# Optimization experiments

Measured on AMD Instinct MI355X. Metric: run time of the kernel, lower is better.

## Reference

```python
import jax, jax.numpy as jnp
import numpy as np

T, B, IN_DIM = 8192, 4, 512
D_V, D_K, CHUNK = 512, 64, 128
EPS = 1e-8


def setup_inputs() -> dict:
    key = jax.random.key(0)
    ks = jax.random.split(key, 9)
    s = 0.02
    return {
        "x": jax.random.normal(ks[0], (T, B, IN_DIM), jnp.float32),
        "Wv": jax.random.normal(ks[1], (D_V, IN_DIM), jnp.float32) * s,
        "bv": jnp.zeros((D_V,), jnp.float32),
        "Wk": jax.random.normal(ks[2], (D_K, IN_DIM), jnp.float32) * s,
        "bk": jnp.zeros((D_K,), jnp.float32),
        "Wq": jax.random.normal(ks[3], (D_K, IN_DIM), jnp.float32) * s,
        "bq": jnp.zeros((D_K,), jnp.float32),
        "Wa": jax.random.normal(ks[4], (D_K, IN_DIM), jnp.float32) * s,
        "ba": jnp.zeros((D_K,), jnp.float32),
    }


def reference(x, Wv, bv, Wk, bk, Wq, bq, Wa, ba):
    # Projections: x (T, B, in_dim)
    v = x @ Wv.T + bv                      # (T, B, d)
    k = x @ Wk.T + bk                      # (T, B, n)
    q = x @ Wq.T + bq                      # (T, B, n)
    alpha = jax.nn.sigmoid(x @ Wa.T + ba)  # (T, B, n) decay gates

    Tt, Bb = x.shape[0], x.shape[1]
    C = CHUNK
    nC = Tt // C  # T assumed divisible by chunk size

    def to_chunks(a):
        return a.reshape(nC, C, Bb, a.shape[-1])

    vs, ks_, qs, als = to_chunks(v), to_chunks(k), to_chunks(q), to_chunks(alpha)
    causal = jnp.tril(jnp.ones((C, C), dtype=bool))  # (C, C)

    def body(S, inp):
        v_ch, k_ch, q_ch, a_ch = inp  # each (C, B, .)
        # Cumulative decay product within chunk (clamped as in the original)
        p = jnp.cumprod(jnp.maximum(a_ch, EPS), axis=0)      # (C, B, n)
        q_t = q_ch * p                                        # (C, B, n)
        k_t = k_ch / (p + EPS)                                # (C, B, n)
        # Intra-chunk causal attention scores
        A = jnp.einsum('tbn,sbn->bts', q_t, k_t)              # (B, C, C)
        A = jnp.where(causal[None, :, :], A, jnp.zeros((), A.dtype))
        y = jnp.einsum('bts,sbd->tbd', A, v_ch)               # intra-chunk
        y = y + jnp.einsum('bdn,tbn->tbd', S, q_t)            # cross-chunk carry
        # State update to end of chunk
        p_end = p[-1]                                         # (B, n)
        S_writes = jnp.einsum('tbd,tbn->bdn', v_ch, k_t * p_end[None, :, :])
        S_new = S * p_end[:, None, :] + S_writes              # (B, d, n)
        return S_new, y

    S0 = jnp.zeros((Bb, D_V, D_K), x.dtype)
    _, ys = jax.lax.scan(body, S0, (vs, ks_, qs, als))        # ys: (nC, C, B, d)
    return ys.reshape(Tt, Bb, D_V)
```

## Files before the change

### kernel.cpp

```cpp
#include <hip/hip_runtime.h>
#include <math.h>

#define T_DIM 8192
#define B_DIM 4
#define INDIM 512
#define DV 512
#define DK 64
#define CHUNK 128
#define NCH (T_DIM / CHUNK)
#define ROWS (T_DIM * B_DIM)
#define NPAD 768
#define KCAT 192
#define EPSF 1e-8f

typedef float float4_t __attribute__((ext_vector_type(4)));
typedef short short8_t __attribute__((ext_vector_type(8)));
typedef _Float16 half8_t __attribute__((ext_vector_type(8)));

__device__ inline unsigned short f2bf(float f) {
  unsigned int u = __float_as_uint(f);
  unsigned int r = (u + 0x7fffu + ((u >> 16) & 1u)) >> 16;
  return (unsigned short)r;
}
__device__ inline float bf2f(unsigned short h) {
  return __uint_as_float(((unsigned int)h) << 16);
}
__device__ inline unsigned short f2h(float f) {
  _Float16 h = (_Float16)f;
  unsigned short u;
  __builtin_memcpy(&u, &h, 2);
  return u;
}

__device__ inline void gload16(const void* g, void* l) {
  __builtin_amdgcn_global_load_lds(
      (const __attribute__((address_space(1))) void*)g,
      (__attribute__((address_space(3))) void*)l, 16, 0, 0);
}

__global__ __launch_bounds__(256) void cast_kernel(
    const float* __restrict__ x,
    const float* __restrict__ Wv, const float* __restrict__ Wk,
    const float* __restrict__ Wq, const float* __restrict__ Wa,
    const float* __restrict__ bv, const float* __restrict__ bk,
    const float* __restrict__ bq, const float* __restrict__ ba,
    unsigned short* __restrict__ xh, unsigned short* __restrict__ wh,
    float* __restrict__ bcat)
{
  if (blockIdx.x < 16384) {
    const size_t i4 = ((size_t)blockIdx.x * 256 + threadIdx.x) * 4;
    const float4 v = *(const float4*)&x[i4];
    ushort4 h;
    h.x = f2h(v.x); h.y = f2h(v.y); h.z = f2h(v.z); h.w = f2h(v.w);
    *(ushort4*)&xh[i4] = h;
  } else {
    const int t = (blockIdx.x - 16384) * 256 + threadIdx.x;
    const size_t i4 = (size_t)t * 4;
    const int row = (int)(i4 >> 9);
    const int col = (int)(i4 & 511);
    float4 v = {0.f, 0.f, 0.f, 0.f};
    if (row < 512)      v = *(const float4*)&Wv[(size_t)row * INDIM + col];
    else if (row < 576) v = *(const float4*)&Wk[(size_t)(row - 512) * INDIM + col];
    else if (row < 640) v = *(const float4*)&Wq[(size_t)(row - 576) * INDIM + col];
    else if (row < 704) v = *(const float4*)&Wa[(size_t)(row - 640) * INDIM + col];
    ushort4 h;
    h.x = f2h(v.x); h.y = f2h(v.y); h.z = f2h(v.z); h.w = f2h(v.w);
    *(ushort4*)&wh[i4] = h;
    if (t < NPAD) {
      float b = 0.f;
      if (t < 512)      b = bv[t];
      else if (t < 576) b = bk[t - 512];
      else if (t < 640) b = bq[t - 576];
      else if (t < 704) b = ba[t - 640];
      bcat[t] = b;
    }
  }
}

__global__ __launch_bounds__(256) void proj_mfma_kernel(
    const unsigned short* __restrict__ xh, const unsigned short* __restrict__ wh,
    const float* __restrict__ bcat,
    unsigned short* __restrict__ Bt_h, unsigned short* __restrict__ Bt_l,
    float* __restrict__ k_ws, float* __restrict__ q_ws,
    float* __restrict__ a_ws)
{
  __shared__ __align__(16) _Float16 Ah[3][128 * 32];
  __shared__ __align__(16) _Float16 Bh[3][128 * 32];

  const int d     = blockIdx.x;
  const int grp   = d >> 3;
  const int ytile = (d & 7) * 32 + grp / 6;
  const int xtile = grp % 6;
  const int r0 = ytile * 128;
  const int c0 = xtile * 128;

  const int tid  = threadIdx.x;
  const int wave = tid >> 6, lane = tid & 63;
  const int wm   = (wave & 1) * 64, wn = (wave >> 1) * 64;
  const int fm   = lane & 15;
  const int fk   = (lane >> 4) * 8;
  const int g    = lane >> 4;

  float4_t acc[4][4];
#pragma unroll
  for (int i = 0; i < 4; ++i)
#pragma unroll
    for (int j = 0; j < 4; ++j) acc[i][j] = (float4_t)0.0f;

  const int srow = tid >> 2;
  const int scol = (tid & 3) * 8;

  const unsigned short* pA0 = xh + (size_t)(r0 + srow) * INDIM + scol;
  const unsigned short* pA1 = xh + (size_t)(r0 + 64 + srow) * INDIM + scol;
  const unsigned short* pB0 = wh + (size_t)(c0 + srow) * INDIM + scol;
  const unsigned short* pB1 = wh + (size_t)(c0 + 64 + srow) * INDIM + scol;

  auto stage = [&](int buf, int k0) {
    gload16(pA0 + k0, &Ah[buf][tid * 8]);
    gload16(pA1 + k0, &Ah[buf][(256 + tid) * 8]);
    gload16(pB0 + k0, &Bh[buf][tid * 8]);
    gload16(pB1 + k0, &Bh[buf][(256 + tid) * 8]);
  };

  auto compute = [&](int buf) {
    half8_t a[4], b[4];
#pragma unroll
    for (int i = 0; i < 4; ++i)
      a[i] = *(const half8_t*)&Ah[buf][(wm + i * 16 + fm) * 32 + fk];
#pragma unroll
    for (int j = 0; j < 4; ++j)
      b[j] = *(const half8_t*)&Bh[buf][(wn + j * 16 + fm) * 32 + fk];
    __builtin_amdgcn_s_setprio(1);
#pragma unroll
    for (int i = 0; i < 4; ++i)
#pragma unroll
      for (int j = 0; j < 4; ++j)
        acc[i][j] = __builtin_amdgcn_mfma_f32_16x16x32_f16(a[i], b[j], acc[i][j], 0, 0, 0);
    __builtin_amdgcn_s_setprio(0);
  };

  stage(0, 0);
  stage(1, 32);
  int cur = 0;
  for (int t = 0; t < 14; ++t) {
    stage((cur + 2) % 3, (t + 2) * 32);
    asm volatile("s_waitcnt vmcnt(8)" ::: "memory");
    __builtin_amdgcn_s_barrier();
    compute(cur);
    __builtin_amdgcn_s_barrier();
    cur = (cur + 1) % 3;
  }
  asm volatile("s_waitcnt vmcnt(4)" ::: "memory");
  __builtin_amdgcn_s_barrier();
  compute(cur);
  cur = (cur + 1) % 3;
  asm volatile("s_waitcnt vmcnt(0)" ::: "memory");
  __builtin_amdgcn_s_barrier();
  compute(cur);

  if (xtile < 4) {
    unsigned int* Thl = (unsigned int*)&Ah[0][0];
    const int t0 = r0 >> 2;
    const int cb0 = (t0 >> 7) * 4;
    const int s0 = t0 & 127;
    __syncthreads();
    for (int bb = 0; bb < 4; ++bb) {
#pragma unroll
      for (int j = 0; j < 4; ++j) {
        const int d_loc = wn + j * 16 + fm;
        const float bias = bcat[c0 + d_loc];
#pragma unroll
        for (int i = 0; i < 4; ++i) {
          const int trow = (wm >> 2) + i * 4 + g;
          const float val = acc[i][j][bb] + bias;
          const unsigned short h = f2bf(val);
          const unsigned short l = f2bf(val - bf2f(h));
          Thl[d_loc * 34 + trow] = (unsigned int)h | ((unsigned int)l << 16);
        }
      }
      __syncthreads();
#pragma unroll
      for (int q2 = 0; q2 < 4; ++q2) {
        const int task = q2 * 256 + tid;
        const int dd = task >> 3;
        const int tq = task & 7;
        const unsigned int* p = &Thl[dd * 34 + tq * 4];
        const unsigned int w0 = p[0], w1 = p[1], w2 = p[2], w3 = p[3];
        ushort4 hh, ll;
        hh.x = (unsigned short)w0; ll.x = (unsigned short)(w0 >> 16);
        hh.y = (unsigned short)w1; ll.y = (unsigned short)(w1 >> 16);
        hh.z = (unsigned short)w2; ll.z = (unsigned short)(w2 >> 16);
        hh.w = (unsigned short)w3; ll.w = (unsigned short)(w3 >> 16);
        const size_t oa = ((size_t)(cb0 + bb) * DV + c0 + dd) * CHUNK + s0 + tq * 4;
        *(ushort4*)&Bt_h[oa] = hh;
        *(ushort4*)&Bt_l[oa] = ll;
      }
      __syncthreads();
    }
  } else {
#pragma unroll
    for (int j = 0; j < 4; ++j) {
      const int col = c0 + wn + j * 16 + fm;
      if (col >= 704) continue;
      const float bias = bcat[col];
#pragma unroll
      for (int i = 0; i < 4; ++i) {
#pragma unroll
        for (int r = 0; r < 4; ++r) {
          const int row = r0 + wm + i * 16 + g * 4 + r;
          const float val = acc[i][j][r] + bias;
          if (col < 576) {
            k_ws[(size_t)row * DK + col - 512] = val;
          } else if (col < 640) {
            q_ws[(size_t)row * DK + col - 576] = val;
          } else {
            a_ws[(size_t)row * DK + col - 640] = 1.0f / (1.0f + expf(-val));
          }
        }
      }
    }
  }
}

__global__ __launch_bounds__(512) void prep_kernel(
    const float* __restrict__ a_ws, const float* __restrict__ k_ws,
    const float* __restrict__ q_ws,
    unsigned short* __restrict__ Acat_h, unsigned short* __restrict__ Acat_l,
    unsigned short* __restrict__ kT_h, unsigned short* __restrict__ kT_l,
    float* __restrict__ pend)
{
  __shared__ float pal[CHUNK][DK];
  __shared__ __align__(16) unsigned short Aq_h[128 * 64];
  __shared__ __align__(16) unsigned short Aq_l[128 * 64];
  __shared__ __align__(16) unsigned short Bk_h[128 * 64];
  __shared__ __align__(16) unsigned short Bk_l[128 * 64];

  const int c = blockIdx.x, b = blockIdx.y;
  const int cb = c * B_DIM + b;
  const int tid = threadIdx.x;
  const int wave = tid >> 6, lane = tid & 63;
  const int wm = (wave & 1) * 64, wn = (wave >> 1) * 32;
  const int fm = lane & 15;
  const int fk = (lane >> 4) * 8;
  const int g  = lane >> 4;

#pragma unroll
  for (int i = 0; i < 4; ++i) {
    const int f = (i * 512 + tid) * 4;
    const int t = f >> 6, n0 = f & 63;
    const float4 av = *(const float4*)&a_ws[(size_t)(c * CHUNK + t) * 256 + b * 64 + n0];
    *(float4*)&pal[t][n0] = av;
  }
  __syncthreads();

  if (tid < 64) {
    float p = 1.0f;
#pragma unroll 4
    for (int t = 0; t < CHUNK; ++t) {
      p *= fmaxf(pal[t][tid], EPSF);
      pal[t][tid] = p;
    }
    pend[c * 256 + b * 64 + tid] = p;
  }
  __syncthreads();

#pragma unroll
  for (int i = 0; i < 4; ++i) {
    const int f = (i * 512 + tid) * 4;
    const int t = f >> 6, n0 = f & 63;
    const float4 qv = *(const float4*)&q_ws[(size_t)(c * CHUNK + t) * 256 + b * 64 + n0];
    const size_t qa = ((size_t)cb * CHUNK + t) * KCAT + 128 + n0;
    float q0 = qv.x * pal[t][n0 + 0];
    float q1 = qv.y * pal[t][n0 + 1];
    float q2 = qv.z * pal[t][n0 + 2];
    float q3 = qv.w * pal[t][n0 + 3];
    ushort4 h, l;
    h.x = f2bf(q0); l.x = f2bf(q0 - bf2f(h.x));
    h.y = f2bf(q1); l.y = f2bf(q1 - bf2f(h.y));
    h.z = f2bf(q2); l.z = f2bf(q2 - bf2f(h.z));
    h.w = f2bf(q3); l.w = f2bf(q3 - bf2f(h.w));
    *(ushort4*)&Acat_h[qa] = h;
    *(ushort4*)&Acat_l[qa] = l;
    const int wi = t * 64 + (n0 ^ ((t & 7) << 3));
    *(ushort4*)&Aq_h[wi] = h;
    *(ushort4*)&Aq_l[wi] = l;
  }

#pragma unroll
  for (int i = 0; i < 4; ++i) {
    const int f = (i * 512 + tid) * 4;
    const int t = f >> 6, n0 = f & 63;
    const float4 kv = *(const float4*)&k_ws[(size_t)(c * CHUNK + t) * 256 + b * 64 + n0];
    float k0 = kv.x / (pal[t][n0 + 0] + EPSF);
    float k1 = kv.y / (pal[t][n0 + 1] + EPSF);
    float k2 = kv.z / (pal[t][n0 + 2] + EPSF);
    float k3 = kv.w / (pal[t][n0 + 3] + EPSF);
    ushort4 h, l;
    h.x = f2bf(k0); l.x = f2bf(k0 - bf2f(h.x));
    h.y = f2bf(k1); l.y = f2bf(k1 - bf2f(h.y));
    h.z = f2bf(k2); l.z = f2bf(k2 - bf2f(h.z));
    h.w = f2bf(k3); l.w = f2bf(k3 - bf2f(h.w));
    const int wi = t * 64 + (n0 ^ ((t & 7) << 3));
    *(ushort4*)&Bk_h[wi] = h;
    *(ushort4*)&Bk_l[wi] = l;
  }
  __syncthreads();

#pragma unroll
  for (int it = 0; it < 2; ++it) {
    const int task = it * 512 + tid;
    const int n  = task >> 4;
    const int tg = task & 15;
    ushort4 h0, h1, l0, l1;
    unsigned short hh[8], ll[8];
#pragma unroll
    for (int e = 0; e < 8; ++e) {
      const int wi = (tg * 8 + e) * 64 + (n ^ (e << 3));
      hh[e] = Bk_h[wi];
      ll[e] = Bk_l[wi];
    }
    h0.x = hh[0]; h0.y = hh[1]; h0.z = hh[2]; h0.w = hh[3];
    h1.x = hh[4]; h1.y = hh[5]; h1.z = hh[6]; h1.w = hh[7];
    l0.x = ll[0]; l0.y = ll[1]; l0.z = ll[2]; l0.w = ll[3];
    l1.x = ll[4]; l1.y = ll[5]; l1.z = ll[6]; l1.w = ll[7];
    const size_t oa = ((size_t)cb * DK + n) * CHUNK + tg * 8;
    *(ushort4*)&kT_h[oa]     = h0;
    *(ushort4*)&kT_h[oa + 4] = h1;
    *(ushort4*)&kT_l[oa]     = l0;
    *(ushort4*)&kT_l[oa + 4] = l1;
  }

  float4_t acc[4][2];
#pragma unroll
  for (int i = 0; i < 4; ++i)
#pragma unroll
    for (int j = 0; j < 2; ++j) acc[i][j] = (float4_t)0.0f;

#pragma unroll
  for (int ksub = 0; ksub < 2; ++ksub) {
    short8_t a_hi[4], a_lo[4], b_hi[2], b_lo[2];
#pragma unroll
    for (int i = 0; i < 4; ++i) {
      const int r = wm + i * 16 + fm;
      const int ar = r * 64 + ((ksub * 32 + fk) ^ ((r & 7) << 3));
      a_hi[i] = *(const short8_t*)&Aq_h[ar];
      a_lo[i] = *(const short8_t*)&Aq_l[ar];
    }
#pragma unroll
    for (int j = 0; j < 2; ++j) {
      const int r = wn + j * 16 + fm;
      const int br = r * 64 + ((ksub * 32 + fk) ^ ((r & 7) << 3));
      b_hi[j] = *(const short8_t*)&Bk_h[br];
      b_lo[j] = *(const short8_t*)&Bk_l[br];
    }
    __builtin_amdgcn_s_setprio(1);
#pragma unroll
    for (int i = 0; i < 4; ++i)
#pragma unroll
      for (int j = 0; j < 2; ++j) {
        acc[i][j] = __builtin_amdgcn_mfma_f32_16x16x32_bf16(a_hi[i], b_hi[j], acc[i][j], 0, 0, 0);
        acc[i][j] = __builtin_amdgcn_mfma_f32_16x16x32_bf16(a_lo[i], b_hi[j], acc[i][j], 0, 0, 0);
        acc[i][j] = __builtin_amdgcn_mfma_f32_16x16x32_bf16(a_hi[i], b_lo[j], acc[i][j], 0, 0, 0);
      }
    __builtin_amdgcn_s_setprio(0);
  }

#pragma unroll
  for (int j = 0; j < 2; ++j) {
    const int s = wn + j * 16 + fm;
#pragma unroll
    for (int i = 0; i < 4; ++i) {
#pragma unroll
      for (int r = 0; r < 4; ++r) {
        const int t = wm + i * 16 + g * 4 + r;
        const float vv = (s <= t) ? acc[i][j][r] : 0.0f;
        const unsigned short h = f2bf(vv);
        const size_t oa = ((size_t)cb * CHUNK + t) * KCAT + s;
        Acat_h[oa] = h;
        Acat_l[oa] = f2bf(vv - bf2f(h));
      }
    }
  }
}

__global__ __launch_bounds__(256) void wchunk_mfma_kernel(
    const unsigned short* __restrict__ Bt_h, const unsigned short* __restrict__ Bt_l,
    const unsigned short* __restrict__ kT_h, const unsigned short* __restrict__ kT_l,
    const float* __restrict__ pend, float* __restrict__ W_ws)
{
  __shared__ __align__(16) unsigned short Ah[128 * 32];
  __shared__ __align__(16) unsigned short Al[128 * 32];
  __shared__ __align__(16) unsigned short Kh[64 * 128];
  __shared__ __align__(16) unsigned short Kl[64 * 128];

  const int bd = blockIdx.x;
  const int cb = (bd >> 5) * 8 + (bd & 7);
  const int dt = (bd >> 3) & 3;
  const int c = cb >> 2, b = cb & 3;
  (void)c; (void)b;
  const int tid  = threadIdx.x;
  const int wave = tid >> 6, lane = tid & 63;
  const int wm   = (wave & 1) * 64;
  const int wn   = (wave >> 1) * 32;
  const int fm   = lane & 15;
  const int fk   = (lane >> 4) * 8;

  const unsigned short* Ab_h = Bt_h + ((size_t)cb * DV + dt * 128) * CHUNK;
  const unsigned short* Ab_l = Bt_l + ((size_t)cb * DV + dt * 128) * CHUNK;
  const unsigned short* Kb_h = kT_h + (size_t)cb * DK * CHUNK;
  const unsigned short* Kb_l = kT_l + (size_t)cb * DK * CHUNK;

#pragma unroll
  for (int it = 0; it < 4; ++it) {
    const int tk = it * 256 + tid;
    const int n = tk >> 4, slot = tk & 15;
    gload16(&Kb_h[(size_t)n * CHUNK + ((slot ^ (n & 15)) << 3)], &Kh[tk * 8]);
    gload16(&Kb_l[(size_t)n * CHUNK + ((slot ^ (n & 15)) << 3)], &Kl[tk * 8]);
  }

  float4_t acc[4][2];
#pragma unroll
  for (int i = 0; i < 4; ++i)
#pragma unroll
    for (int j = 0; j < 2; ++j) acc[i][j] = (float4_t)0.0f;

  for (int ks = 0; ks < 4; ++ks) {
    const int k0 = ks * 32;
#pragma unroll
    for (int q = 0; q < 2; ++q) {
      const int flat = (q * 256 + tid) * 8;
      const int row = flat >> 5, col = flat & 31;
      gload16(&Ab_h[(size_t)row * CHUNK + k0 + col], &Ah[flat]);
      gload16(&Ab_l[(size_t)row * CHUNK + k0 + col], &Al[flat]);
    }
    __syncthreads();

    short8_t a_hi[4], a_lo[4], b_hi[2], b_lo[2];
#pragma unroll
    for (int i = 0; i < 4; ++i) {
      const int ar = (wm + i * 16 + fm) * 32 + fk;
      a_hi[i] = *(const short8_t*)&Ah[ar];
      a_lo[i] = *(const short8_t*)&Al[ar];
    }
#pragma unroll
    for (int j = 0; j < 2; ++j) {
      const int n = wn + j * 16 + fm;
      const int slot = (k0 + fk) >> 3;
      const int addr = n * CHUNK + ((slot ^ (n & 15)) << 3);
      b_hi[j] = *(const short8_t*)&Kh[addr];
      b_lo[j] = *(const short8_t*)&Kl[addr];
    }
#pragma unroll
    for (int i = 0; i < 4; ++i)
#pragma unroll
      for (int j = 0; j < 2; ++j) {
        acc[i][j] = __builtin_amdgcn_mfma_f32_16x16x32_bf16(a_hi[i], b_hi[j], acc[i][j], 0, 0, 0);
        acc[i][j] = __builtin_amdgcn_mfma_f32_16x16x32_bf16(a_lo[i], b_hi[j], acc[i][j], 0, 0, 0);
        acc[i][j] = __builtin_amdgcn_mfma_f32_16x16x32_bf16(a_hi[i], b_lo[j], acc[i][j], 0, 0, 0);
      }
    __syncthreads();
  }

#pragma unroll
  for (int j = 0; j < 2; ++j) {
    const int n = wn + j * 16 + fm;
    const float pj = pend[(cb >> 2) * 256 + (cb & 3) * 64 + n];
#pragma unroll
    for (int i = 0; i < 4; ++i) {
#pragma unroll
      for (int r = 0; r < 4; ++r) {
        const int dd = dt * 128 + wm + i * 16 + (lane >> 4) * 4 + r;
        W_ws[((size_t)cb * DV + dd) * DK + n] = acc[i][j][r] * pj;
      }
    }
  }
}

__global__ __launch_bounds__(256) void scan_kernel(
    const float* __restrict__ W_ws, const float* __restrict__ pend,
    unsigned short* __restrict__ Sh, unsigned short* __restrict__ Sl)
{
  const int flat = blockIdx.x * 256 + threadIdx.x;
  const int n = flat & 63;
  const int bd = flat >> 6;
  const int b = bd >> 9;
  float s = 0.0f;
  for (int c = 0; c < NCH; ++c) {
    const int off = c * 131072 + flat;
    const float w = W_ws[off];
    const unsigned short h = f2bf(s);
    Sh[off] = h;
    Sl[off] = f2bf(s - bf2f(h));
    s = s * pend[c * 256 + b * 64 + n] + w;
  }
}

__global__ __launch_bounds__(256) void out_mfma_kernel(
    const unsigned short* __restrict__ Acat_h, const unsigned short* __restrict__ Acat_l,
    const unsigned short* __restrict__ Bt_h, const unsigned short* __restrict__ Bt_l,
    const unsigned short* __restrict__ Sh, const unsigned short* __restrict__ Sl,
    float* __restrict__ out)
{
  __shared__ __align__(16) unsigned short Ah[128 * 64];
  __shared__ __align__(16) unsigned short Al[128 * 64];
  __shared__ __align__(16) unsigned short Bh[128 * 64];
  __shared__ __align__(16) unsigned short Bl[128 * 64];

  const int bd = blockIdx.x;
  const int cb = (bd >> 5) * 8 + (bd & 7);
  const int nt = (bd >> 3) & 3;
  const int c = cb >> 2, b = cb & 3;
  const int tid  = threadIdx.x;
  const int wave = tid >> 6, lane = tid & 63;
  const int wm   = (wave & 1) * 64, wn = (wave >> 1) * 64;
  const int fm   = lane & 15;
  const int fk   = (lane >> 4) * 8;

  const unsigned short* Ab_h = Acat_h + (size_t)cb * CHUNK * KCAT;
  const unsigned short* Ab_l = Acat_l + (size_t)cb * CHUNK * KCAT;
  const unsigned short* Bb_h = Bt_h + ((size_t)cb * DV + nt * 128) * CHUNK;
  const unsigned short* Bb_l = Bt_l + ((size_t)cb * DV + nt * 128) * CHUNK;
  const unsigned short* Sb_h = Sh + ((size_t)cb * DV + nt * 128) * DK;
  const unsigned short* Sb_l = Sl + ((size_t)cb * DV + nt * 128) * DK;

  const int srow = tid >> 3;
  const int scolB = (tid & 7) * 16;
  const int sc = (scolB ^ ((srow & 7) << 4)) >> 1;
  const int sdst = srow * 64 + (scolB >> 1);

  float4_t acc[4][4];
#pragma unroll
  for (int i = 0; i < 4; ++i)
#pragma unroll
    for (int j = 0; j < 4; ++j) acc[i][j] = (float4_t)0.0f;

  for (int ks = 0; ks < 3; ++ks) {
    const int k0 = ks * 64;
#pragma unroll
    for (int q = 0; q < 4; ++q) {
      const int row = q * 32 + srow;
      const int dst = q * 2048 + sdst;
      gload16(&Ab_h[(size_t)row * KCAT + k0 + sc], &Ah[dst]);
      gload16(&Ab_l[(size_t)row * KCAT + k0 + sc], &Al[dst]);
      if (ks < 2) {
        gload16(&Bb_h[(size_t)row * CHUNK + k0 + sc], &Bh[dst]);
        gload16(&Bb_l[(size_t)row * CHUNK + k0 + sc], &Bl[dst]);
      } else {
        gload16(&Sb_h[(size_t)row * DK + sc], &Bh[dst]);
        gload16(&Sb_l[(size_t)row * DK + sc], &Bl[dst]);
      }
    }
    __syncthreads();

#pragma unroll
    for (int ksub = 0; ksub < 2; ++ksub) {
      short8_t a_hi[4], a_lo[4], b_hi[4], b_lo[4];
#pragma unroll
      for (int i = 0; i < 4; ++i) {
        const int r = wm + i * 16 + fm;
        const int ar = r * 64 + ((ksub * 32 + fk) ^ ((r & 7) << 3));
        a_hi[i] = *(const short8_t*)&Ah[ar];
        a_lo[i] = *(const short8_t*)&Al[ar];
      }
#pragma unroll
      for (int j = 0; j < 4; ++j) {
        const int r = wn + j * 16 + fm;
        const int br = r * 64 + ((ksub * 32 + fk) ^ ((r & 7) << 3));
        b_hi[j] = *(const short8_t*)&Bh[br];
        b_lo[j] = *(const short8_t*)&Bl[br];
      }
      __builtin_amdgcn_s_setprio(1);
#pragma unroll
      for (int i = 0; i < 4; ++i)
#pragma unroll
        for (int j = 0; j < 4; ++j) {
          acc[i][j] = __builtin_amdgcn_mfma_f32_16x16x32_bf16(a_hi[i], b_hi[j], acc[i][j], 0, 0, 0);
          acc[i][j] = __builtin_amdgcn_mfma_f32_16x16x32_bf16(a_lo[i], b_hi[j], acc[i][j], 0, 0, 0);
          acc[i][j] = __builtin_amdgcn_mfma_f32_16x16x32_bf16(a_hi[i], b_lo[j], acc[i][j], 0, 0, 0);
        }
      __builtin_amdgcn_s_setprio(0);
    }
    __syncthreads();
  }

#pragma unroll
  for (int j = 0; j < 4; ++j) {
    const int d = nt * 128 + wn + j * 16 + fm;
#pragma unroll
    for (int i = 0; i < 4; ++i) {
#pragma unroll
      for (int r = 0; r < 4; ++r) {
        const int t = c * CHUNK + wm + i * 16 + (lane >> 4) * 4 + r;
        out[((size_t)t * B_DIM + b) * DV + d] = acc[i][j][r];
      }
    }
  }
}

extern "C" void kernel_launch(void* const* d_in, const int* in_sizes, int n_in,
                              void* d_out, int out_size, void* d_ws, size_t ws_size,
                              hipStream_t stream)
{
  const float* x  = (const float*)d_in[0];
  const float* Wv = (const float*)d_in[1];
  const float* bv = (const float*)d_in[2];
  const float* Wk = (const float*)d_in[3];
  const float* bk = (const float*)d_in[4];
  const float* Wq = (const float*)d_in[5];
  const float* bq = (const float*)d_in[6];
  const float* Wa = (const float*)d_in[7];
  const float* ba = (const float*)d_in[8];
  float* out = (float*)d_out;

  float* ws   = (float*)d_ws;
  unsigned short* Bt_h = (unsigned short*)ws;
  unsigned short* Bt_l = Bt_h + (size_t)NCH * B_DIM * DV * CHUNK;
  float* k_ws = ws + (size_t)ROWS * DV;
  float* a_ws = k_ws + (size_t)ROWS * DK;
  float* pend = a_ws + (size_t)ROWS * DK;
  float* W_ws = pend + NCH * B_DIM * DK;
  float* bcat = W_ws + (size_t)NCH * B_DIM * DV * DK;
  unsigned short* Acat_h = (unsigned short*)(bcat + NPAD);
  unsigned short* Acat_l = Acat_h + (size_t)NCH * B_DIM * CHUNK * KCAT;
  unsigned short* uni = Acat_l + (size_t)NCH * B_DIM * CHUNK * KCAT;
  unsigned short* xh = uni;
  unsigned short* wh = xh + (size_t)ROWS * INDIM;
  float* q_ws = (float*)(uni + (size_t)18 * 1024 * 1024);
  unsigned short* kT_h = (unsigned short*)(q_ws + (size_t)ROWS * DK);
  unsigned short* kT_l = kT_h + (size_t)NCH * B_DIM * DK * CHUNK;
  unsigned short* S_h = uni;
  unsigned short* S_l = S_h + (size_t)NCH * B_DIM * DV * DK;

  cast_kernel<<<16384 + 384, 256, 0, stream>>>(
      x, Wv, Wk, Wq, Wa, bv, bk, bq, ba, xh, wh, bcat);
  proj_mfma_kernel<<<(ROWS / 128) * (NPAD / 128), 256, 0, stream>>>(
      xh, wh, bcat, Bt_h, Bt_l, k_ws, q_ws, a_ws);
  prep_kernel<<<dim3(NCH, B_DIM), 512, 0, stream>>>(
      a_ws, k_ws, q_ws, Acat_h, Acat_l, kT_h, kT_l, pend);
  wchunk_mfma_kernel<<<NCH * B_DIM * 4, 256, 0, stream>>>(
      Bt_h, Bt_l, kT_h, kT_l, pend, W_ws);
  scan_kernel<<<(B_DIM * DV * DK) / 256, 256, 0, stream>>>(
      W_ws, pend, S_h, S_l);
  out_mfma_kernel<<<NCH * B_DIM * 4, 256, 0, stream>>>(
      Acat_h, Acat_l, Bt_h, Bt_l, S_h, S_l, out);
}
```

Measured before the change: 260.1 us.

## Fuse fp32-to-fp16 cast of x into projection GEMM's A-tile loader

```diff
diff --git a/kernel.cpp b/kernel.cpp
--- a/kernel.cpp
+++ b/kernel.cpp
@@ -38,47 +38,37 @@
       (__attribute__((address_space(3))) void*)l, 16, 0, 0);
 }
 
-__global__ __launch_bounds__(256) void cast_kernel(
-    const float* __restrict__ x,
+__global__ __launch_bounds__(256) void wcast_kernel(
     const float* __restrict__ Wv, const float* __restrict__ Wk,
     const float* __restrict__ Wq, const float* __restrict__ Wa,
     const float* __restrict__ bv, const float* __restrict__ bk,
     const float* __restrict__ bq, const float* __restrict__ ba,
-    unsigned short* __restrict__ xh, unsigned short* __restrict__ wh,
-    float* __restrict__ bcat)
+    unsigned short* __restrict__ wh, float* __restrict__ bcat)
 {
-  if (blockIdx.x < 16384) {
-    const size_t i4 = ((size_t)blockIdx.x * 256 + threadIdx.x) * 4;
-    const float4 v = *(const float4*)&x[i4];
-    ushort4 h;
-    h.x = f2h(v.x); h.y = f2h(v.y); h.z = f2h(v.z); h.w = f2h(v.w);
-    *(ushort4*)&xh[i4] = h;
-  } else {
-    const int t = (blockIdx.x - 16384) * 256 + threadIdx.x;
-    const size_t i4 = (size_t)t * 4;
-    const int row = (int)(i4 >> 9);
-    const int col = (int)(i4 & 511);
-    float4 v = {0.f, 0.f, 0.f, 0.f};
-    if (row < 512)      v = *(const float4*)&Wv[(size_t)row * INDIM + col];
-    else if (row < 576) v = *(const float4*)&Wk[(size_t)(row - 512) * INDIM + col];
-    else if (row < 640) v = *(const float4*)&Wq[(size_t)(row - 576) * INDIM + col];
-    else if (row < 704) v = *(const float4*)&Wa[(size_t)(row - 640) * INDIM + col];
-    ushort4 h;
-    h.x = f2h(v.x); h.y = f2h(v.y); h.z = f2h(v.z); h.w = f2h(v.w);
-    *(ushort4*)&wh[i4] = h;
-    if (t < NPAD) {
-      float b = 0.f;
-      if (t < 512)      b = bv[t];
-      else if (t < 576) b = bk[t - 512];
-      else if (t < 640) b = bq[t - 576];
-      else if (t < 704) b = ba[t - 640];
-      bcat[t] = b;
-    }
+  const int t = blockIdx.x * 256 + threadIdx.x;
+  const size_t i4 = (size_t)t * 4;
+  const int row = (int)(i4 >> 9);
+  const int col = (int)(i4 & 511);
+  float4 v = {0.f, 0.f, 0.f, 0.f};
+  if (row < 512)      v = *(const float4*)&Wv[(size_t)row * INDIM + col];
+  else if (row < 576) v = *(const float4*)&Wk[(size_t)(row - 512) * INDIM + col];
+  else if (row < 640) v = *(const float4*)&Wq[(size_t)(row - 576) * INDIM + col];
+  else if (row < 704) v = *(const float4*)&Wa[(size_t)(row - 640) * INDIM + col];
+  ushort4 h;
+  h.x = f2h(v.x); h.y = f2h(v.y); h.z = f2h(v.z); h.w = f2h(v.w);
+  *(ushort4*)&wh[i4] = h;
+  if (t < NPAD) {
+    float b = 0.f;
+    if (t < 512)      b = bv[t];
+    else if (t < 576) b = bk[t - 512];
+    else if (t < 640) b = bq[t - 576];
+    else if (t < 704) b = ba[t - 640];
+    bcat[t] = b;
   }
 }
 
 __global__ __launch_bounds__(256) void proj_mfma_kernel(
-    const unsigned short* __restrict__ xh, const unsigned short* __restrict__ wh,
+    const float* __restrict__ x, const unsigned short* __restrict__ wh,
     const float* __restrict__ bcat,
     unsigned short* __restrict__ Bt_h, unsigned short* __restrict__ Bt_l,
     float* __restrict__ k_ws, float* __restrict__ q_ws,
@@ -110,18 +100,38 @@
   const int srow = tid >> 2;
   const int scol = (tid & 3) * 8;
 
-  const unsigned short* pA0 = xh + (size_t)(r0 + srow) * INDIM + scol;
-  const unsigned short* pA1 = xh + (size_t)(r0 + 64 + srow) * INDIM + scol;
+  const float* pX0 = x + (size_t)(r0 + srow) * INDIM + scol;
+  const float* pX1 = x + (size_t)(r0 + 64 + srow) * INDIM + scol;
   const unsigned short* pB0 = wh + (size_t)(c0 + srow) * INDIM + scol;
   const unsigned short* pB1 = wh + (size_t)(c0 + 64 + srow) * INDIM + scol;
 
-  auto stage = [&](int buf, int k0) {
-    gload16(pA0 + k0, &Ah[buf][tid * 8]);
-    gload16(pA1 + k0, &Ah[buf][(256 + tid) * 8]);
+  float4 ra0[4], ra1[4];
+
+  auto loadA = [&](float4* ra, int kt) {
+    const int k0 = kt * 32;
+    ra[0] = *(const float4*)(pX0 + k0);
+    ra[1] = *(const float4*)(pX0 + k0 + 4);
+    ra[2] = *(const float4*)(pX1 + k0);
+    ra[3] = *(const float4*)(pX1 + k0 + 4);
+  };
+  auto writeA = [&](const float4* ra, int buf) {
+    half8_t h0, h1;
+    h0[0] = (_Float16)ra[0].x; h0[1] = (_Float16)ra[0].y;
+    h0[2] = (_Float16)ra[0].z; h0[3] = (_Float16)ra[0].w;
+    h0[4] = (_Float16)ra[1].x; h0[5] = (_Float16)ra[1].y;
+    h0[6] = (_Float16)ra[1].z; h0[7] = (_Float16)ra[1].w;
+    h1[0] = (_Float16)ra[2].x; h1[1] = (_Float16)ra[2].y;
+    h1[2] = (_Float16)ra[2].z; h1[3] = (_Float16)ra[2].w;
+    h1[4] = (_Float16)ra[3].x; h1[5] = (_Float16)ra[3].y;
+    h1[6] = (_Float16)ra[3].z; h1[7] = (_Float16)ra[3].w;
+    *(half8_t*)&Ah[buf][tid * 8] = h0;
+    *(half8_t*)&Ah[buf][(256 + tid) * 8] = h1;
+  };
+  auto stageB = [&](int buf, int kt) {
+    const int k0 = kt * 32;
     gload16(pB0 + k0, &Bh[buf][tid * 8]);
     gload16(pB1 + k0, &Bh[buf][(256 + tid) * 8]);
   };
-
   auto compute = [&](int buf) {
     half8_t a[4], b[4];
 #pragma unroll
@@ -139,24 +149,27 @@
     __builtin_amdgcn_s_setprio(0);
   };
 
-  stage(0, 0);
-  stage(1, 32);
-  int cur = 0;
-  for (int t = 0; t < 14; ++t) {
-    stage((cur + 2) % 3, (t + 2) * 32);
-    asm volatile("s_waitcnt vmcnt(8)" ::: "memory");
-    __builtin_amdgcn_s_barrier();
-    compute(cur);
-    __builtin_amdgcn_s_barrier();
-    cur = (cur + 1) % 3;
-  }
-  asm volatile("s_waitcnt vmcnt(4)" ::: "memory");
-  __builtin_amdgcn_s_barrier();
-  compute(cur);
-  cur = (cur + 1) % 3;
-  asm volatile("s_waitcnt vmcnt(0)" ::: "memory");
-  __builtin_amdgcn_s_barrier();
-  compute(cur);
+  loadA(ra0, 0);
+  stageB(0, 0);
+  loadA(ra1, 1);
+  stageB(1, 1);
+
+#define PSTEP(T, RA)                                                       \
+  {                                                                        \
+    if ((T) < 15) asm volatile("s_waitcnt vmcnt(6)" ::: "memory");         \
+    else          asm volatile("s_waitcnt vmcnt(0)" ::: "memory");         \
+    writeA(RA, (T) % 3);                                                   \
+    if ((T) + 2 < 16) { loadA(RA, (T) + 2); stageB(((T) + 2) % 3, (T) + 2); } \
+    asm volatile("s_waitcnt lgkmcnt(0)" ::: "memory");                     \
+    __builtin_amdgcn_s_barrier();                                          \
+    compute((T) % 3);                                                      \
+    __builtin_amdgcn_s_barrier();                                          \
+  }
+  PSTEP(0, ra0)  PSTEP(1, ra1)  PSTEP(2, ra0)  PSTEP(3, ra1)
+  PSTEP(4, ra0)  PSTEP(5, ra1)  PSTEP(6, ra0)  PSTEP(7, ra1)
+  PSTEP(8, ra0)  PSTEP(9, ra1)  PSTEP(10, ra0) PSTEP(11, ra1)
+  PSTEP(12, ra0) PSTEP(13, ra1) PSTEP(14, ra0) PSTEP(15, ra1)
+#undef PSTEP
 
   if (xtile < 4) {
     unsigned int* Thl = (unsigned int*)&Ah[0][0];
@@ -180,20 +193,25 @@
       }
       __syncthreads();
 #pragma unroll
-      for (int q2 = 0; q2 < 4; ++q2) {
+      for (int q2 = 0; q2 < 2; ++q2) {
         const int task = q2 * 256 + tid;
-        const int dd = task >> 3;
-        const int tq = task & 7;
-        const unsigned int* p = &Thl[dd * 34 + tq * 4];
+        const int dd = task >> 2;
+        const int tq = task & 3;
+        const unsigned int* p = &Thl[dd * 34 + tq * 8];
         const unsigned int w0 = p[0], w1 = p[1], w2 = p[2], w3 = p[3];
-        ushort4 hh, ll;
-        hh.x = (unsigned short)w0; ll.x = (unsigned short)(w0 >> 16);
-        hh.y = (unsigned short)w1; ll.y = (unsigned short)(w1 >> 16);
-        hh.z = (unsigned short)w2; ll.z = (unsigned short)(w2 >> 16);
-        hh.w = (unsigned short)w3; ll.w = (unsigned short)(w3 >> 16);
-        const size_t oa = ((size_t)(cb0 + bb) * DV + c0 + dd) * CHUNK + s0 + tq * 4;
-        *(ushort4*)&Bt_h[oa] = hh;
-        *(ushort4*)&Bt_l[oa] = ll;
+        const unsigned int w4 = p[4], w5 = p[5], w6 = p[6], w7 = p[7];
+        uint4 hv, lv;
+        hv.x = (w0 & 0xffffu) | (w1 << 16);
+        hv.y = (w2 & 0xffffu) | (w3 << 16);
+        hv.z = (w4 & 0xffffu) | (w5 << 16);
+        hv.w = (w6 & 0xffffu) | (w7 << 16);
+        lv.x = (w0 >> 16) | (w1 & 0xffff0000u);
+        lv.y = (w2 >> 16) | (w3 & 0xffff0000u);
+        lv.z = (w4 >> 16) | (w5 & 0xffff0000u);
+        lv.w = (w6 >> 16) | (w7 & 0xffff0000u);
+        const size_t oa = ((size_t)(cb0 + bb) * DV + c0 + dd) * CHUNK + s0 + tq * 8;
+        *(uint4*)&Bt_h[oa] = hv;
+        *(uint4*)&Bt_l[oa] = lv;
       }
       __syncthreads();
     }
@@ -396,8 +414,6 @@
   const int bd = blockIdx.x;
   const int cb = (bd >> 5) * 8 + (bd & 7);
   const int dt = (bd >> 3) & 3;
-  const int c = cb >> 2, b = cb & 3;
-  (void)c; (void)b;
   const int tid  = threadIdx.x;
   const int wave = tid >> 6, lane = tid & 63;
   const int wm   = (wave & 1) * 64;
@@ -623,18 +639,17 @@
   unsigned short* Acat_h = (unsigned short*)(bcat + NPAD);
   unsigned short* Acat_l = Acat_h + (size_t)NCH * B_DIM * CHUNK * KCAT;
   unsigned short* uni = Acat_l + (size_t)NCH * B_DIM * CHUNK * KCAT;
-  unsigned short* xh = uni;
-  unsigned short* wh = xh + (size_t)ROWS * INDIM;
+  unsigned short* S_h = uni;
+  unsigned short* S_l = S_h + (size_t)NCH * B_DIM * DV * DK;
+  unsigned short* wh = uni + (size_t)ROWS * INDIM;
   float* q_ws = (float*)(uni + (size_t)18 * 1024 * 1024);
   unsigned short* kT_h = (unsigned short*)(q_ws + (size_t)ROWS * DK);
   unsigned short* kT_l = kT_h + (size_t)NCH * B_DIM * DK * CHUNK;
-  unsigned short* S_h = uni;
-  unsigned short* S_l = S_h + (size_t)NCH * B_DIM * DV * DK;
-
-  cast_kernel<<<16384 + 384, 256, 0, stream>>>(
-      x, Wv, Wk, Wq, Wa, bv, bk, bq, ba, xh, wh, bcat);
+
+  wcast_kernel<<<384, 256, 0, stream>>>(
+      Wv, Wk, Wq, Wa, bv, bk, bq, ba, wh, bcat);
   proj_mfma_kernel<<<(ROWS / 128) * (NPAD / 128), 256, 0, stream>>>(
-      xh, wh, bcat, Bt_h, Bt_l, k_ws, q_ws, a_ws);
+      x, wh, bcat, Bt_h, Bt_l, k_ws, q_ws, a_ws);
   prep_kernel<<<dim3(NCH, B_DIM), 512, 0, stream>>>(
       a_ws, k_ws, q_ws, Acat_h, Acat_l, kT_h, kT_l, pend);
   wchunk_mfma_kernel<<<NCH * B_DIM * 4, 256, 0, stream>>>(
```

Result: slower. 284.3 us (+9.3%).
